# Kernel optimization log

Measured on AMD Instinct MI355X. Metric: run time of the kernel, lower is better.

The kernel has to match this reference:

```python
import jax, jax.numpy as jnp
import numpy as np

N_EMBD = 1024
N_HEAD = 16
HEAD_DIM = N_EMBD // N_HEAD


def setup_inputs() -> dict:
    key = jax.random.key(0)
    k1, k2, k3, k4, k5 = jax.random.split(key, 5)
    B, T, C = 4, 2048, N_EMBD
    s = 0.02
    return {
        "x": jax.random.normal(k1, (B, T, C), dtype=jnp.float32),
        "w_qkv": jax.random.normal(k2, (C, 3 * C), dtype=jnp.float32) * s,
        "b_qkv": jnp.zeros((3 * C,), dtype=jnp.float32),
        "w_proj": jax.random.normal(k3, (C, C), dtype=jnp.float32) * s,
        "b_proj": jnp.zeros((C,), dtype=jnp.float32),
    }


def reference(x, w_qkv, b_qkv, w_proj, b_proj):
    B, T, C = x.shape
    H, D = N_HEAD, HEAD_DIM
    qkv = x @ w_qkv + b_qkv                      # [B,T,3C]
    q, k, v = jnp.split(qkv, 3, axis=2)
    q = q.reshape(B, T, H, D).transpose(0, 2, 1, 3)  # [B,H,T,D]
    k = k.reshape(B, T, H, D).transpose(0, 2, 1, 3)
    v = v.reshape(B, T, H, D).transpose(0, 2, 1, 3)
    att = jnp.einsum("bhqd,bhkd->bhqk", q, k) * (1.0 / D ** 0.5)
    causal = jnp.tril(jnp.ones((T, T), dtype=bool))
    att = jnp.where(causal[None, None], att, -jnp.inf)
    att = jax.nn.softmax(att, axis=-1)
    y = jnp.einsum("bhqk,bhkd->bhqd", att, v)    # [B,H,T,D]
    y = y.transpose(0, 2, 1, 3).reshape(B, T, C)
    return y @ w_proj + b_proj
```

## Files before the change

kernel.cpp:

```cpp
#include <hip/hip_runtime.h>
#include <hip/hip_bf16.h>

#define B_ 4
#define T_ 2048
#define C_ 1024
#define H_ 16
#define D_ 64
#define M_ (B_ * T_)
#define N3_ (3 * C_)

typedef __attribute__((ext_vector_type(4))) float f32x4;
typedef __attribute__((ext_vector_type(16))) float f32x16;
typedef __attribute__((ext_vector_type(8))) short bf16x8;

__device__ __forceinline__ ushort f2bf(float f) {
  union { float f; unsigned u; } v; v.f = f;
  unsigned r = v.u + 0x7fffu + ((v.u >> 16) & 1u);
  return (ushort)(r >> 16);
}

__device__ __forceinline__ void gload_lds16(const ushort* g, ushort* l) {
  __builtin_amdgcn_global_load_lds((const __attribute__((address_space(1))) void*)g,
                                   (__attribute__((address_space(3))) void*)l, 16, 0, 0);
}

__device__ __forceinline__ unsigned cvtpk_bf16(float lo, float hi) {
  unsigned r;
  asm("v_cvt_pk_bf16_f32 %0, %1, %2" : "=v"(r) : "v"(lo), "v"(hi));
  return r;
}

__global__ void cvt_bf16_kernel(const float* __restrict__ in, ushort* __restrict__ out, int n4) {
  int i = blockIdx.x * blockDim.x + threadIdx.x;
  int stride = gridDim.x * blockDim.x;
  for (; i < n4; i += stride) {
    float4 v = reinterpret_cast<const float4*>(in)[i];
    ushort4 o;
    o.x = f2bf(v.x); o.y = f2bf(v.y); o.z = f2bf(v.z); o.w = f2bf(v.w);
    reinterpret_cast<ushort4*>(out)[i] = o;
  }
}

__global__ __launch_bounds__(256) void transpose_cvt_kernel(const float* __restrict__ in,
                                                            ushort* __restrict__ out,
                                                            int K, int N) {
  __shared__ float tile[64][65];
  int k0 = blockIdx.y * 64, n0 = blockIdx.x * 64;
  int t = threadIdx.x;
  int rr = t >> 6, cc = t & 63;
#pragma unroll
  for (int i = 0; i < 16; ++i) {
    int r = i * 4 + rr;
    tile[r][cc] = in[(size_t)(k0 + r) * N + n0 + cc];
  }
  __syncthreads();
#pragma unroll
  for (int i = 0; i < 16; ++i) {
    int r = i * 4 + rr;
    out[(size_t)(n0 + r) * K + k0 + cc] = f2bf(tile[cc][r]);
  }
}

__global__ __launch_bounds__(256) void gemm_qkv_kernel(const ushort* __restrict__ A,
                                                       const ushort* __restrict__ Bt,
                                                       const float* __restrict__ bias,
                                                       ushort* __restrict__ qb,
                                                       ushort* __restrict__ kb,
                                                       ushort* __restrict__ vT) {
  __shared__ __align__(16) ushort As[128 * 32];
  __shared__ __align__(16) ushort Bs[128 * 32];
  const int tid = threadIdx.x;
  const int wid = tid >> 6, lane = tid & 63;
  const int wm = wid >> 1, wn = wid & 1;
  const int lr = lane & 15, lg = lane >> 4;
  const int bm = blockIdx.y * 128, bn = blockIdx.x * 128;
  const int srow = wid * 32 + (lane >> 2);
  const int scol = (lane & 3) * 8;
  ushort* lA = &As[wid * 32 * 32];
  ushort* lB = &Bs[wid * 32 * 32];
  const ushort* gA0 = A  + (size_t)(bm + srow) * 1024 + scol;
  const ushort* gB0 = Bt + (size_t)(bn + srow) * 1024 + scol;
  f32x4 acc[4][4] = {};
  for (int k0 = 0; k0 < 1024; k0 += 32) {
    gload_lds16(gA0 + k0, lA);
    gload_lds16(gA0 + k0 + 16 * 1024, lA + 16 * 32);
    gload_lds16(gB0 + k0, lB);
    gload_lds16(gB0 + k0 + 16 * 1024, lB + 16 * 32);
    __syncthreads();
    bf16x8 af[4], bfr[4];
#pragma unroll
    for (int f = 0; f < 4; ++f) {
      af[f]  = *(const bf16x8*)&As[(wm * 64 + f * 16 + lr) * 32 + lg * 8];
      bfr[f] = *(const bf16x8*)&Bs[(wn * 64 + f * 16 + lr) * 32 + lg * 8];
    }
#pragma unroll
    for (int fm = 0; fm < 4; ++fm)
#pragma unroll
      for (int fn = 0; fn < 4; ++fn)
        acc[fm][fn] = __builtin_amdgcn_mfma_f32_16x16x32_bf16(af[fm], bfr[fn], acc[fm][fn], 0, 0, 0);
    __syncthreads();
  }
#pragma unroll
  for (int fm = 0; fm < 4; ++fm)
#pragma unroll
    for (int fn = 0; fn < 4; ++fn) {
      int m0 = bm + wm * 64 + fm * 16 + lg * 4;
      int n  = bn + wn * 64 + fn * 16 + lr;
      float b = bias[n];
      int part = n >> 10, cch = n & 1023;
      int h = cch >> 6, d = cch & 63;
      int bb = m0 >> 11, t = m0 & 2047;
      size_t bh = (size_t)bb * H_ + h;
      if (part == 2) {
        ushort4 pv;
        pv.x = f2bf(acc[fm][fn][0] + b);
        pv.y = f2bf(acc[fm][fn][1] + b);
        pv.z = f2bf(acc[fm][fn][2] + b);
        pv.w = f2bf(acc[fm][fn][3] + b);
        *(ushort4*)&vT[(bh * D_ + d) * T_ + t] = pv;
      } else if (part == 0) {
#pragma unroll
        for (int r = 0; r < 4; ++r)
          qb[(bh * T_ + t + r) * D_ + d] = f2bf((acc[fm][fn][r] + b) * 0.125f);
      } else {
#pragma unroll
        for (int r = 0; r < 4; ++r)
          kb[(bh * T_ + t + r) * D_ + d] = f2bf(acc[fm][fn][r] + b);
      }
    }
}

__global__ __launch_bounds__(256) void gemm_proj_kernel(const ushort* __restrict__ A,
                                                        const ushort* __restrict__ Bt,
                                                        const float* __restrict__ bias,
                                                        float* __restrict__ out) {
  __shared__ __align__(16) ushort As[128 * 32];
  __shared__ __align__(16) ushort Bs[128 * 32];
  const int tid = threadIdx.x;
  const int wid = tid >> 6, lane = tid & 63;
  const int wm = wid >> 1, wn = wid & 1;
  const int lr = lane & 15, lg = lane >> 4;
  const int bm = blockIdx.y * 128, bn = blockIdx.x * 128;
  const int srow = wid * 32 + (lane >> 2);
  const int scol = (lane & 3) * 8;
  ushort* lA = &As[wid * 32 * 32];
  ushort* lB = &Bs[wid * 32 * 32];
  const ushort* gA0 = A  + (size_t)(bm + srow) * 1024 + scol;
  const ushort* gB0 = Bt + (size_t)(bn + srow) * 1024 + scol;
  f32x4 acc[4][4] = {};
  for (int k0 = 0; k0 < 1024; k0 += 32) {
    gload_lds16(gA0 + k0, lA);
    gload_lds16(gA0 + k0 + 16 * 1024, lA + 16 * 32);
    gload_lds16(gB0 + k0, lB);
    gload_lds16(gB0 + k0 + 16 * 1024, lB + 16 * 32);
    __syncthreads();
    bf16x8 af[4], bfr[4];
#pragma unroll
    for (int f = 0; f < 4; ++f) {
      af[f]  = *(const bf16x8*)&As[(wm * 64 + f * 16 + lr) * 32 + lg * 8];
      bfr[f] = *(const bf16x8*)&Bs[(wn * 64 + f * 16 + lr) * 32 + lg * 8];
    }
#pragma unroll
    for (int fm = 0; fm < 4; ++fm)
#pragma unroll
      for (int fn = 0; fn < 4; ++fn)
        acc[fm][fn] = __builtin_amdgcn_mfma_f32_16x16x32_bf16(af[fm], bfr[fn], acc[fm][fn], 0, 0, 0);
    __syncthreads();
  }
#pragma unroll
  for (int fm = 0; fm < 4; ++fm)
#pragma unroll
    for (int fn = 0; fn < 4; ++fn)
#pragma unroll
      for (int r = 0; r < 4; ++r) {
        int m = bm + wm * 64 + fm * 16 + lg * 4 + r;
        int n = bn + wn * 64 + fn * 16 + lr;
        out[(size_t)m * C_ + n] = acc[fm][fn][r] + bias[n];
      }
}

__global__ void attn_kernel(const ushort* __restrict__ qb,
                            const ushort* __restrict__ kb,
                            const ushort* __restrict__ vT,
                            ushort* __restrict__ yb) {
  const int bh = blockIdx.y;
  const int tid = threadIdx.x, wid = tid >> 6, lane = tid & 63;
  const int l31 = lane & 31, hi = lane >> 5;
  const int wj = blockIdx.x * 4 + wid;
  const int bb = bh >> 4, h = bh & 15;
  const ushort* Qb = qb + (size_t)bh * T_ * D_;
  const ushort* Kb = kb + (size_t)bh * T_ * D_;
  const ushort* Vb = vT + (size_t)bh * D_ * T_;
  const ushort* V0 = Vb + (size_t)(0 * 32 + l31) * T_;
  const ushort* V1 = Vb + (size_t)(1 * 32 + l31) * T_;

  const int i = (blockIdx.z == 0) ? wj : 63 - wj;
  const int qr0 = i * 32;
  const int qrow = qr0 + l31;
  const int ntiles = (i >> 1) + 1;
  bf16x8 qf[4];
#pragma unroll
  for (int ds = 0; ds < 4; ++ds)
    qf[ds] = *(const bf16x8*)&Qb[(size_t)qrow * D_ + ds * 16 + 8 * hi];
  f32x16 o0 = {}, o1 = {};
  float mrun = -1e30f, lsum = 0.f;

  for (int tx = 0; tx < ntiles; ++tx) {
    const int k0 = tx * 64;
    bf16x8 kf0[4], kf1[4];
#pragma unroll
    for (int ds = 0; ds < 4; ++ds) {
      kf0[ds] = *(const bf16x8*)&Kb[(size_t)(k0 + l31) * D_ + ds * 16 + 8 * hi];
      kf1[ds] = *(const bf16x8*)&Kb[(size_t)(k0 + 32 + l31) * D_ + ds * 16 + 8 * hi];
    }
    bf16x8 vf0[4], vf1[4];
#pragma unroll
    for (int sl = 0; sl < 4; ++sl) {
      vf0[sl] = *(const bf16x8*)&V0[k0 + sl * 16 + 8 * hi];
      vf1[sl] = *(const bf16x8*)&V1[k0 + sl * 16 + 8 * hi];
    }
    f32x16 s0 = {}, s1 = {};
#pragma unroll
    for (int ds = 0; ds < 4; ++ds) {
      s0 = __builtin_amdgcn_mfma_f32_32x32x16_bf16(kf0[ds], qf[ds], s0, 0, 0, 0);
      s1 = __builtin_amdgcn_mfma_f32_32x32x16_bf16(kf1[ds], qf[ds], s1, 0, 0, 0);
    }
    if (tx == ntiles - 1) {
#pragma unroll
      for (int e = 0; e < 16; ++e) {
        int key = k0 + (e & 3) + 8 * (e >> 2) + 4 * hi;
        if (key > qrow)      s0[e] = -1e30f;
        if (key + 32 > qrow) s1[e] = -1e30f;
      }
    }
    float mx;
    {
      float a0 = fmaxf(fmaxf(s0[0], s0[1]), fmaxf(s0[2], s0[3]));
      float a1 = fmaxf(fmaxf(s0[4], s0[5]), fmaxf(s0[6], s0[7]));
      float a2 = fmaxf(fmaxf(s0[8], s0[9]), fmaxf(s0[10], s0[11]));
      float a3 = fmaxf(fmaxf(s0[12], s0[13]), fmaxf(s0[14], s0[15]));
      float b0 = fmaxf(fmaxf(s1[0], s1[1]), fmaxf(s1[2], s1[3]));
      float b1 = fmaxf(fmaxf(s1[4], s1[5]), fmaxf(s1[6], s1[7]));
      float b2 = fmaxf(fmaxf(s1[8], s1[9]), fmaxf(s1[10], s1[11]));
      float b3 = fmaxf(fmaxf(s1[12], s1[13]), fmaxf(s1[14], s1[15]));
      mx = fmaxf(fmaxf(fmaxf(a0, a1), fmaxf(a2, a3)), fmaxf(fmaxf(b0, b1), fmaxf(b2, b3)));
    }
    float pmax = fmaxf(mx, __shfl_xor(mx, 32));
    if (!__all(pmax - mrun <= 8.f)) {
      float nm = fmaxf(mrun, pmax);
      float sc = __expf(mrun - nm);
#pragma unroll
      for (int e = 0; e < 16; ++e) { o0[e] *= sc; o1[e] *= sc; }
      lsum *= sc;
      mrun = nm;
    }
    float ls0 = 0.f, ls1 = 0.f, ls2 = 0.f, ls3 = 0.f;
#pragma unroll
    for (int e = 0; e < 4; ++e) {
      s0[e]      = __expf(s0[e]      - mrun); ls0 += s0[e];
      s0[e + 4]  = __expf(s0[e + 4]  - mrun); ls1 += s0[e + 4];
      s0[e + 8]  = __expf(s0[e + 8]  - mrun); ls2 += s0[e + 8];
      s0[e + 12] = __expf(s0[e + 12] - mrun); ls3 += s0[e + 12];
    }
#pragma unroll
    for (int e = 0; e < 4; ++e) {
      s1[e]      = __expf(s1[e]      - mrun); ls0 += s1[e];
      s1[e + 4]  = __expf(s1[e + 4]  - mrun); ls1 += s1[e + 4];
      s1[e + 8]  = __expf(s1[e + 8]  - mrun); ls2 += s1[e + 8];
      s1[e + 12] = __expf(s1[e + 12] - mrun); ls3 += s1[e + 12];
    }
    lsum += (ls0 + ls1) + (ls2 + ls3);
    bf16x8 pb[4];
#pragma unroll
    for (int half = 0; half < 2; ++half) {
      const f32x16& sv = half == 0 ? s0 : s1;
#pragma unroll
      for (int ss = 0; ss < 2; ++ss) {
        unsigned u = cvtpk_bf16(sv[ss * 8 + 0], sv[ss * 8 + 1]);
        unsigned v = cvtpk_bf16(sv[ss * 8 + 2], sv[ss * 8 + 3]);
        unsigned w = cvtpk_bf16(sv[ss * 8 + 4], sv[ss * 8 + 5]);
        unsigned z = cvtpk_bf16(sv[ss * 8 + 6], sv[ss * 8 + 7]);
        asm("v_permlane32_swap_b32 %0, %1" : "+v"(u), "+v"(w));
        asm("v_permlane32_swap_b32 %0, %1" : "+v"(v), "+v"(z));
        union { unsigned w4[4]; bf16x8 f; } pk;
        pk.w4[0] = u; pk.w4[1] = v; pk.w4[2] = w; pk.w4[3] = z;
        pb[half * 2 + ss] = pk.f;
      }
    }
#pragma unroll
    for (int sl = 0; sl < 4; ++sl) {
      o0 = __builtin_amdgcn_mfma_f32_32x32x16_bf16(vf0[sl], pb[sl], o0, 0, 0, 0);
      o1 = __builtin_amdgcn_mfma_f32_32x32x16_bf16(vf1[sl], pb[sl], o1, 0, 0, 0);
    }
  }
  float lt = lsum + __shfl_xor(lsum, 32);
  float linv = 1.f / lt;
  ushort* yrow = yb + ((size_t)(bb * T_ + qrow)) * C_ + h * D_;
#pragma unroll
  for (int rg = 0; rg < 4; ++rg) {
    ushort4 w0, w1;
    w0.x = f2bf(o0[rg * 4 + 0] * linv); w0.y = f2bf(o0[rg * 4 + 1] * linv);
    w0.z = f2bf(o0[rg * 4 + 2] * linv); w0.w = f2bf(o0[rg * 4 + 3] * linv);
    w1.x = f2bf(o1[rg * 4 + 0] * linv); w1.y = f2bf(o1[rg * 4 + 1] * linv);
    w1.z = f2bf(o1[rg * 4 + 2] * linv); w1.w = f2bf(o1[rg * 4 + 3] * linv);
    *(ushort4*)&yrow[8 * rg + 4 * hi]      = w0;
    *(ushort4*)&yrow[32 + 8 * rg + 4 * hi] = w1;
  }
}

extern "C" void kernel_launch(void* const* d_in, const int* in_sizes, int n_in,
                              void* d_out, int out_size, void* d_ws, size_t ws_size,
                              hipStream_t stream) {
  const float* x      = (const float*)d_in[0];
  const float* w_qkv  = (const float*)d_in[1];
  const float* b_qkv  = (const float*)d_in[2];
  const float* w_proj = (const float*)d_in[3];
  const float* b_proj = (const float*)d_in[4];
  float* out = (float*)d_out;

  char* ws = (char*)d_ws;
  const size_t MB = 1024 * 1024;
  ushort* xb     = (ushort*)(ws);
  ushort* wqkvT  = (ushort*)(ws + 16 * MB);
  ushort* wprojT = (ushort*)(ws + 22 * MB);
  ushort* qbuf   = (ushort*)(ws + 24 * MB);
  ushort* kbuf   = (ushort*)(ws + 40 * MB);
  ushort* vTbuf  = (ushort*)(ws + 56 * MB);
  ushort* ybuf   = (ushort*)(ws + 72 * MB);

  cvt_bf16_kernel<<<2048, 256, 0, stream>>>(x, xb, M_ * C_ / 4);
  transpose_cvt_kernel<<<dim3(N3_ / 64, C_ / 64), 256, 0, stream>>>(w_qkv, wqkvT, C_, N3_);
  transpose_cvt_kernel<<<dim3(C_ / 64, C_ / 64), 256, 0, stream>>>(w_proj, wprojT, C_, C_);
  gemm_qkv_kernel<<<dim3(N3_ / 128, M_ / 128), 256, 0, stream>>>(xb, wqkvT, b_qkv, qbuf, kbuf, vTbuf);
  attn_kernel<<<dim3(8, B_ * H_, 2), 256, 0, stream>>>(qbuf, kbuf, vTbuf, ybuf);
  gemm_proj_kernel<<<dim3(C_ / 128, M_ / 128), 256, 0, stream>>>(ybuf, wprojT, b_proj, out);
}
```

Measured before the change: 362.7 us.

## Pipeline K loads in attention, pair causal rows per wave, use exp2 with folded scale

Result: faster. 330.3 us (-8.9%).

```diff
diff --git a/kernel.cpp b/kernel.cpp
--- a/kernel.cpp
+++ b/kernel.cpp
@@ -28,6 +28,10 @@
   unsigned r;
   asm("v_cvt_pk_bf16_f32 %0, %1, %2" : "=v"(r) : "v"(lo), "v"(hi));
   return r;
+}
+
+__device__ __forceinline__ float exp2fast(float x) {
+  return __builtin_amdgcn_exp2f(x);
 }
 
 __global__ void cvt_bf16_kernel(const float* __restrict__ in, ushort* __restrict__ out, int n4) {
@@ -61,6 +65,7 @@
   }
 }
 
+#define QSCALE 0.1803368801111244f
 __global__ __launch_bounds__(256) void gemm_qkv_kernel(const ushort* __restrict__ A,
                                                        const ushort* __restrict__ Bt,
                                                        const float* __restrict__ bias,
@@ -121,7 +126,7 @@
       } else if (part == 0) {
 #pragma unroll
         for (int r = 0; r < 4; ++r)
-          qb[(bh * T_ + t + r) * D_ + d] = f2bf((acc[fm][fn][r] + b) * 0.125f);
+          qb[(bh * T_ + t + r) * D_ + d] = f2bf((acc[fm][fn][r] + b) * QSCALE);
       } else {
 #pragma unroll
         for (int r = 0; r < 4; ++r)
@@ -179,133 +184,139 @@
       }
 }
 
-__global__ void attn_kernel(const ushort* __restrict__ qb,
-                            const ushort* __restrict__ kb,
-                            const ushort* __restrict__ vT,
-                            ushort* __restrict__ yb) {
-  const int bh = blockIdx.y;
+__global__ __launch_bounds__(256, 2) void attn_kernel(const ushort* __restrict__ qb,
+                                                      const ushort* __restrict__ kb,
+                                                      const ushort* __restrict__ vT,
+                                                      ushort* __restrict__ yb) {
+  const int bh = blockIdx.x;
   const int tid = threadIdx.x, wid = tid >> 6, lane = tid & 63;
   const int l31 = lane & 31, hi = lane >> 5;
-  const int wj = blockIdx.x * 4 + wid;
+  const int wj = blockIdx.y * 4 + wid;
   const int bb = bh >> 4, h = bh & 15;
   const ushort* Qb = qb + (size_t)bh * T_ * D_;
   const ushort* Kb = kb + (size_t)bh * T_ * D_;
   const ushort* Vb = vT + (size_t)bh * D_ * T_;
-  const ushort* V0 = Vb + (size_t)(0 * 32 + l31) * T_;
-  const ushort* V1 = Vb + (size_t)(1 * 32 + l31) * T_;
-
-  const int i = (blockIdx.z == 0) ? wj : 63 - wj;
-  const int qr0 = i * 32;
-  const int qrow = qr0 + l31;
-  const int ntiles = (i >> 1) + 1;
-  bf16x8 qf[4];
-#pragma unroll
-  for (int ds = 0; ds < 4; ++ds)
-    qf[ds] = *(const bf16x8*)&Qb[(size_t)qrow * D_ + ds * 16 + 8 * hi];
-  f32x16 o0 = {}, o1 = {};
-  float mrun = -1e30f, lsum = 0.f;
-
-  for (int tx = 0; tx < ntiles; ++tx) {
-    const int k0 = tx * 64;
-    bf16x8 kf0[4], kf1[4];
-#pragma unroll
-    for (int ds = 0; ds < 4; ++ds) {
-      kf0[ds] = *(const bf16x8*)&Kb[(size_t)(k0 + l31) * D_ + ds * 16 + 8 * hi];
-      kf1[ds] = *(const bf16x8*)&Kb[(size_t)(k0 + 32 + l31) * D_ + ds * 16 + 8 * hi];
-    }
-    bf16x8 vf0[4], vf1[4];
-#pragma unroll
-    for (int sl = 0; sl < 4; ++sl) {
-      vf0[sl] = *(const bf16x8*)&V0[k0 + sl * 16 + 8 * hi];
-      vf1[sl] = *(const bf16x8*)&V1[k0 + sl * 16 + 8 * hi];
-    }
-    f32x16 s0 = {}, s1 = {};
-#pragma unroll
-    for (int ds = 0; ds < 4; ++ds) {
-      s0 = __builtin_amdgcn_mfma_f32_32x32x16_bf16(kf0[ds], qf[ds], s0, 0, 0, 0);
-      s1 = __builtin_amdgcn_mfma_f32_32x32x16_bf16(kf1[ds], qf[ds], s1, 0, 0, 0);
-    }
-    if (tx == ntiles - 1) {
-#pragma unroll
-      for (int e = 0; e < 16; ++e) {
-        int key = k0 + (e & 3) + 8 * (e >> 2) + 4 * hi;
-        if (key > qrow)      s0[e] = -1e30f;
-        if (key + 32 > qrow) s1[e] = -1e30f;
+  const ushort* V0 = Vb + (size_t)(l31) * T_;
+  const ushort* V1 = Vb + (size_t)(32 + l31) * T_;
+
+#define LOADK(TX, KF0, KF1)                                                        \
+  do {                                                                             \
+    const int kk_ = (TX) * 64;                                                     \
+    _Pragma("unroll") for (int ds_ = 0; ds_ < 4; ++ds_) {                          \
+      KF0[ds_] = *(const bf16x8*)&Kb[(size_t)(kk_ + l31) * D_ + ds_ * 16 + 8 * hi];      \
+      KF1[ds_] = *(const bf16x8*)&Kb[(size_t)(kk_ + 32 + l31) * D_ + ds_ * 16 + 8 * hi]; \
+    }                                                                              \
+  } while (0)
+
+#define COMPUTE(TX, KF0, KF1)                                                      \
+  do {                                                                             \
+    const int k0_ = (TX) * 64;                                                     \
+    bf16x8 vf0_[4], vf1_[4];                                                       \
+    _Pragma("unroll") for (int sl_ = 0; sl_ < 4; ++sl_) {                          \
+      vf0_[sl_] = *(const bf16x8*)&V0[k0_ + sl_ * 16 + 8 * hi];                    \
+      vf1_[sl_] = *(const bf16x8*)&V1[k0_ + sl_ * 16 + 8 * hi];                    \
+    }                                                                              \
+    f32x16 s0 = {}, s1 = {};                                                       \
+    _Pragma("unroll") for (int ds_ = 0; ds_ < 4; ++ds_) {                          \
+      s0 = __builtin_amdgcn_mfma_f32_32x32x16_bf16(KF0[ds_], qf[ds_], s0, 0, 0, 0);\
+      s1 = __builtin_amdgcn_mfma_f32_32x32x16_bf16(KF1[ds_], qf[ds_], s1, 0, 0, 0);\
+    }                                                                              \
+    if ((TX) == ntiles - 1) {                                                      \
+      _Pragma("unroll") for (int e = 0; e < 16; ++e) {                             \
+        int key = k0_ + (e & 3) + 8 * (e >> 2) + 4 * hi;                           \
+        if (key > qrow)      s0[e] = -1e30f;                                       \
+        if (key + 32 > qrow) s1[e] = -1e30f;                                       \
+      }                                                                            \
+    }                                                                              \
+    float mx;                                                                      \
+    {                                                                              \
+      float a0 = fmaxf(fmaxf(s0[0], s0[1]), fmaxf(s0[2], s0[3]));                  \
+      float a1 = fmaxf(fmaxf(s0[4], s0[5]), fmaxf(s0[6], s0[7]));                  \
+      float a2 = fmaxf(fmaxf(s0[8], s0[9]), fmaxf(s0[10], s0[11]));                \
+      float a3 = fmaxf(fmaxf(s0[12], s0[13]), fmaxf(s0[14], s0[15]));              \
+      float b0 = fmaxf(fmaxf(s1[0], s1[1]), fmaxf(s1[2], s1[3]));                  \
+      float b1 = fmaxf(fmaxf(s1[4], s1[5]), fmaxf(s1[6], s1[7]));                  \
+      float b2 = fmaxf(fmaxf(s1[8], s1[9]), fmaxf(s1[10], s1[11]));                \
+      float b3 = fmaxf(fmaxf(s1[12], s1[13]), fmaxf(s1[14], s1[15]));              \
+      mx = fmaxf(fmaxf(fmaxf(a0, a1), fmaxf(a2, a3)),                              \
+                 fmaxf(fmaxf(b0, b1), fmaxf(b2, b3)));                             \
+    }                                                                              \
+    float pmax = fmaxf(mx, __shfl_xor(mx, 32));                                    \
+    if (!__all(pmax - mrun <= 8.f)) {                                              \
+      float nm = fmaxf(mrun, pmax);                                                \
+      float sc = exp2fast(mrun - nm);                                              \
+      _Pragma("unroll") for (int e = 0; e < 16; ++e) { o0[e] *= sc; o1[e] *= sc; } \
+      lsum *= sc;                                                                  \
+      mrun = nm;                                                                   \
+    }                                                                              \
+    float ls_ = 0.f;                                                               \
+    _Pragma("unroll") for (int e = 0; e < 16; ++e) {                               \
+      s0[e] = exp2fast(s0[e] - mrun); ls_ += s0[e];                                \
+      s1[e] = exp2fast(s1[e] - mrun); ls_ += s1[e];                                \
+    }                                                                              \
+    lsum += ls_;                                                                   \
+    bf16x8 pb[4];                                                                  \
+    _Pragma("unroll") for (int half = 0; half < 2; ++half) {                       \
+      const f32x16& sv = half == 0 ? s0 : s1;                                      \
+      _Pragma("unroll") for (int ss = 0; ss < 2; ++ss) {                           \
+        unsigned u = cvtpk_bf16(sv[ss * 8 + 0], sv[ss * 8 + 1]);                   \
+        unsigned v = cvtpk_bf16(sv[ss * 8 + 2], sv[ss * 8 + 3]);                   \
+        unsigned w = cvtpk_bf16(sv[ss * 8 + 4], sv[ss * 8 + 5]);                   \
+        unsigned z = cvtpk_bf16(sv[ss * 8 + 6], sv[ss * 8 + 7]);                   \
+        asm("v_permlane32_swap_b32 %0, %1" : "+v"(u), "+v"(w));                    \
+        asm("v_permlane32_swap_b32 %0, %1" : "+v"(v), "+v"(z));                    \
+        union { unsigned w4[4]; bf16x8 f; } pk;                                    \
+        pk.w4[0] = u; pk.w4[1] = v; pk.w4[2] = w; pk.w4[3] = z;                    \
+        pb[half * 2 + ss] = pk.f;                                                  \
+      }                                                                            \
+    }                                                                              \
+    _Pragma("unroll") for (int sl_ = 0; sl_ < 4; ++sl_) {                          \
+      o0 = __builtin_amdgcn_mfma_f32_32x32x16_bf16(vf0_[sl_], pb[sl_], o0, 0, 0, 0);\
+      o1 = __builtin_amdgcn_mfma_f32_32x32x16_bf16(vf1_[sl_], pb[sl_], o1, 0, 0, 0);\
+    }                                                                              \
+  } while (0)
+
+  for (int pass = 0; pass < 2; ++pass) {
+    const int i = (pass == 0) ? wj : 63 - wj;
+    const int qrow = i * 32 + l31;
+    const int ntiles = (i >> 1) + 1;
+    bf16x8 qf[4];
+#pragma unroll
+    for (int ds = 0; ds < 4; ++ds)
+      qf[ds] = *(const bf16x8*)&Qb[(size_t)qrow * D_ + ds * 16 + 8 * hi];
+    f32x16 o0 = {}, o1 = {};
+    float mrun = -1e30f, lsum = 0.f;
+
+    bf16x8 kA0[4], kA1[4], kB0[4], kB1[4];
+    LOADK(0, kA0, kA1);
+    int tx = 0;
+    while (tx < ntiles) {
+      if (tx + 1 < ntiles) LOADK(tx + 1, kB0, kB1);
+      COMPUTE(tx, kA0, kA1);
+      ++tx;
+      if (tx < ntiles) {
+        if (tx + 1 < ntiles) LOADK(tx + 1, kA0, kA1);
+        COMPUTE(tx, kB0, kB1);
+        ++tx;
       }
     }
-    float mx;
-    {
-      float a0 = fmaxf(fmaxf(s0[0], s0[1]), fmaxf(s0[2], s0[3]));
-      float a1 = fmaxf(fmaxf(s0[4], s0[5]), fmaxf(s0[6], s0[7]));
-      float a2 = fmaxf(fmaxf(s0[8], s0[9]), fmaxf(s0[10], s0[11]));
-      float a3 = fmaxf(fmaxf(s0[12], s0[13]), fmaxf(s0[14], s0[15]));
-      float b0 = fmaxf(fmaxf(s1[0], s1[1]), fmaxf(s1[2], s1[3]));
-      float b1 = fmaxf(fmaxf(s1[4], s1[5]), fmaxf(s1[6], s1[7]));
-      float b2 = fmaxf(fmaxf(s1[8], s1[9]), fmaxf(s1[10], s1[11]));
-      float b3 = fmaxf(fmaxf(s1[12], s1[13]), fmaxf(s1[14], s1[15]));
-      mx = fmaxf(fmaxf(fmaxf(a0, a1), fmaxf(a2, a3)), fmaxf(fmaxf(b0, b1), fmaxf(b2, b3)));
-    }
-    float pmax = fmaxf(mx, __shfl_xor(mx, 32));
-    if (!__all(pmax - mrun <= 8.f)) {
-      float nm = fmaxf(mrun, pmax);
-      float sc = __expf(mrun - nm);
-#pragma unroll
-      for (int e = 0; e < 16; ++e) { o0[e] *= sc; o1[e] *= sc; }
-      lsum *= sc;
-      mrun = nm;
-    }
-    float ls0 = 0.f, ls1 = 0.f, ls2 = 0.f, ls3 = 0.f;
-#pragma unroll
-    for (int e = 0; e < 4; ++e) {
-      s0[e]      = __expf(s0[e]      - mrun); ls0 += s0[e];
-      s0[e + 4]  = __expf(s0[e + 4]  - mrun); ls1 += s0[e + 4];
-      s0[e + 8]  = __expf(s0[e + 8]  - mrun); ls2 += s0[e + 8];
-      s0[e + 12] = __expf(s0[e + 12] - mrun); ls3 += s0[e + 12];
-    }
-#pragma unroll
-    for (int e = 0; e < 4; ++e) {
-      s1[e]      = __expf(s1[e]      - mrun); ls0 += s1[e];
-      s1[e + 4]  = __expf(s1[e + 4]  - mrun); ls1 += s1[e + 4];
-      s1[e + 8]  = __expf(s1[e + 8]  - mrun); ls2 += s1[e + 8];
-      s1[e + 12] = __expf(s1[e + 12] - mrun); ls3 += s1[e + 12];
-    }
-    lsum += (ls0 + ls1) + (ls2 + ls3);
-    bf16x8 pb[4];
-#pragma unroll
-    for (int half = 0; half < 2; ++half) {
-      const f32x16& sv = half == 0 ? s0 : s1;
-#pragma unroll
-      for (int ss = 0; ss < 2; ++ss) {
-        unsigned u = cvtpk_bf16(sv[ss * 8 + 0], sv[ss * 8 + 1]);
-        unsigned v = cvtpk_bf16(sv[ss * 8 + 2], sv[ss * 8 + 3]);
-        unsigned w = cvtpk_bf16(sv[ss * 8 + 4], sv[ss * 8 + 5]);
-        unsigned z = cvtpk_bf16(sv[ss * 8 + 6], sv[ss * 8 + 7]);
-        asm("v_permlane32_swap_b32 %0, %1" : "+v"(u), "+v"(w));
-        asm("v_permlane32_swap_b32 %0, %1" : "+v"(v), "+v"(z));
-        union { unsigned w4[4]; bf16x8 f; } pk;
-        pk.w4[0] = u; pk.w4[1] = v; pk.w4[2] = w; pk.w4[3] = z;
-        pb[half * 2 + ss] = pk.f;
-      }
-    }
-#pragma unroll
-    for (int sl = 0; sl < 4; ++sl) {
-      o0 = __builtin_amdgcn_mfma_f32_32x32x16_bf16(vf0[sl], pb[sl], o0, 0, 0, 0);
-      o1 = __builtin_amdgcn_mfma_f32_32x32x16_bf16(vf1[sl], pb[sl], o1, 0, 0, 0);
-    }
-  }
-  float lt = lsum + __shfl_xor(lsum, 32);
-  float linv = 1.f / lt;
-  ushort* yrow = yb + ((size_t)(bb * T_ + qrow)) * C_ + h * D_;
-#pragma unroll
-  for (int rg = 0; rg < 4; ++rg) {
-    ushort4 w0, w1;
-    w0.x = f2bf(o0[rg * 4 + 0] * linv); w0.y = f2bf(o0[rg * 4 + 1] * linv);
-    w0.z = f2bf(o0[rg * 4 + 2] * linv); w0.w = f2bf(o0[rg * 4 + 3] * linv);
-    w1.x = f2bf(o1[rg * 4 + 0] * linv); w1.y = f2bf(o1[rg * 4 + 1] * linv);
-    w1.z = f2bf(o1[rg * 4 + 2] * linv); w1.w = f2bf(o1[rg * 4 + 3] * linv);
-    *(ushort4*)&yrow[8 * rg + 4 * hi]      = w0;
-    *(ushort4*)&yrow[32 + 8 * rg + 4 * hi] = w1;
-  }
+
+    float lt = lsum + __shfl_xor(lsum, 32);
+    float linv = 1.f / lt;
+    ushort* yrow = yb + ((size_t)(bb * T_ + qrow)) * C_ + h * D_;
+#pragma unroll
+    for (int rg = 0; rg < 4; ++rg) {
+      ushort4 w0, w1;
+      w0.x = f2bf(o0[rg * 4 + 0] * linv); w0.y = f2bf(o0[rg * 4 + 1] * linv);
+      w0.z = f2bf(o0[rg * 4 + 2] * linv); w0.w = f2bf(o0[rg * 4 + 3] * linv);
+      w1.x = f2bf(o1[rg * 4 + 0] * linv); w1.y = f2bf(o1[rg * 4 + 1] * linv);
+      w1.z = f2bf(o1[rg * 4 + 2] * linv); w1.w = f2bf(o1[rg * 4 + 3] * linv);
+      *(ushort4*)&yrow[8 * rg + 4 * hi]      = w0;
+      *(ushort4*)&yrow[32 + 8 * rg + 4 * hi] = w1;
+    }
+  }
+#undef LOADK
+#undef COMPUTE
 }
 
 extern "C" void kernel_launch(void* const* d_in, const int* in_sizes, int n_in,
@@ -332,6 +343,6 @@
   transpose_cvt_kernel<<<dim3(N3_ / 64, C_ / 64), 256, 0, stream>>>(w_qkv, wqkvT, C_, N3_);
   transpose_cvt_kernel<<<dim3(C_ / 64, C_ / 64), 256, 0, stream>>>(w_proj, wprojT, C_, C_);
   gemm_qkv_kernel<<<dim3(N3_ / 128, M_ / 128), 256, 0, stream>>>(xb, wqkvT, b_qkv, qbuf, kbuf, vTbuf);
-  attn_kernel<<<dim3(8, B_ * H_, 2), 256, 0, stream>>>(qbuf, kbuf, vTbuf, ybuf);
+  attn_kernel<<<dim3(B_ * H_, 8), 256, 0, stream>>>(qbuf, kbuf, vTbuf, ybuf);
   gemm_proj_kernel<<<dim3(C_ / 128, M_ / 128), 256, 0, stream>>>(ybuf, wprojT, b_proj, out);
 }
```
